# Optimization experiments

Hardware: AMD Instinct MI355X
Metric: run time of the kernel (lower is better)

The kernel has to match this reference:

```python
import jax, jax.numpy as jnp
import numpy as np

B, S, D, H = 2, 2048, 1024, 16
HD = D // H
NEG = -10000000000.0

def setup_inputs() -> dict:
    key = jax.random.key(0)
    ks = jax.random.split(key, 9)
    s = 1.0 / np.sqrt(D)
    return {
        "x": jax.random.normal(ks[0], (B, S, D), dtype=jnp.float32),
        "Wq": jax.random.uniform(ks[1], (D, D), jnp.float32, -s, s),
        "bq": jax.random.uniform(ks[2], (D,), jnp.float32, -s, s),
        "Wk": jax.random.uniform(ks[3], (D, D), jnp.float32, -s, s),
        "bk": jax.random.uniform(ks[4], (D,), jnp.float32, -s, s),
        "Wv": jax.random.uniform(ks[5], (D, D), jnp.float32, -s, s),
        "bv": jax.random.uniform(ks[6], (D,), jnp.float32, -s, s),
        "Wo": jax.random.uniform(ks[7], (D, D), jnp.float32, -s, s),
        "bo": jax.random.uniform(ks[8], (D,), jnp.float32, -s, s),
    }

def reference(x, Wq, bq, Wk, bk, Wv, bv, Wo, bo):
    b, s, _ = x.shape
    def split_heads(t):
        return t.reshape(b, s, H, HD).transpose(0, 2, 1, 3)  # [b,h,s,hd]
    Q = split_heads(x @ Wq + bq)
    K = split_heads(x @ Wk + bk)
    V = split_heads(x @ Wv + bv)
    scores = jnp.einsum('bhqd,bhkd->bhqk', Q, K) / jnp.sqrt(jnp.float32(HD))
    causal = jnp.tril(jnp.ones((s, s), dtype=bool))
    scores = jnp.where(causal[None, None], scores, NEG)
    attn = jax.nn.softmax(scores, axis=-1)
    ctx = jnp.einsum('bhqk,bhkd->bhqd', attn, V)
    ctx = ctx.transpose(0, 2, 1, 3).reshape(b, s, D)
    return ctx @ Wo + bo
```

## Files before the change

### kernel.cpp

```cpp
#include <hip/hip_runtime.h>
#include <hip/hip_bf16.h>

#define BB 2
#define SS 2048
#define DD 1024
#define HH 16
#define HD 64
#define MM (BB*SS)

typedef __attribute__((ext_vector_type(8))) short bf16x8;
typedef __attribute__((ext_vector_type(4))) float f32x4;
typedef __attribute__((ext_vector_type(16))) float f32x16;

#define QSCALE 0.18033688f

static __device__ __forceinline__ unsigned short f2bf(float f) {
    unsigned int u = __builtin_bit_cast(unsigned int, f);
    u += 0x7fffu + ((u >> 16) & 1u);
    return (unsigned short)(u >> 16);
}

static __device__ __forceinline__ void gload16(const unsigned short* g, unsigned short* l) {
    __builtin_amdgcn_global_load_lds(
        (const __attribute__((address_space(1))) unsigned int*)g,
        (__attribute__((address_space(3))) unsigned int*)l, 16, 0, 0);
}

__global__ __launch_bounds__(256) void prep_kernel(const float* __restrict__ x,
                                                   const float* __restrict__ W0,
                                                   const float* __restrict__ W1,
                                                   const float* __restrict__ W2,
                                                   const float* __restrict__ W3,
                                                   unsigned short* __restrict__ xb,
                                                   unsigned short* __restrict__ Wt)
{
    const int t = threadIdx.x;
    const int bid = blockIdx.x;
    if (bid < 2048) {
        const size_t i = ((size_t)bid * 256 + t) * 8;
        float4 a = *(const float4*)(x + i);
        float4 b = *(const float4*)(x + i + 4);
        union { unsigned short u[8]; bf16x8 v; } pk;
        pk.u[0] = f2bf(a.x); pk.u[1] = f2bf(a.y); pk.u[2] = f2bf(a.z); pk.u[3] = f2bf(a.w);
        pk.u[4] = f2bf(b.x); pk.u[5] = f2bf(b.y); pk.u[6] = f2bf(b.z); pk.u[7] = f2bf(b.w);
        *(bf16x8*)(xb + i) = pk.v;
        return;
    }
    __shared__ unsigned short Ts[64][72];
    const int wsel = (bid - 2048) >> 8;
    const int rem  = (bid - 2048) & 255;
    const float* W = wsel == 0 ? W0 : wsel == 1 ? W1 : wsel == 2 ? W2 : W3;
    unsigned short* out = Wt + (size_t)wsel * DD * DD;
    const int n0 = (rem & 15) * 64, k0 = (rem >> 4) * 64;
#pragma unroll
    for (int i = 0; i < 4; ++i) {
        const int r = (t >> 4) + i * 16;
        const int c = (t & 15) * 4;
        float4 v = *(const float4*)(W + (size_t)(k0 + r) * DD + n0 + c);
        Ts[c + 0][r] = f2bf(v.x); Ts[c + 1][r] = f2bf(v.y);
        Ts[c + 2][r] = f2bf(v.z); Ts[c + 3][r] = f2bf(v.w);
    }
    __syncthreads();
#pragma unroll
    for (int j = 0; j < 2; ++j) {
        const int ch = j * 256 + t;
        const int rn = ch >> 3, ck = (ch & 7) * 8;
        bf16x8 v = *(const bf16x8*)&Ts[rn][ck];
        *(bf16x8*)(out + (size_t)(n0 + rn) * DD + k0 + ck) = v;
    }
}

__global__ __launch_bounds__(256) void gemm_mfma(const unsigned short* __restrict__ A,
                                                 const unsigned short* __restrict__ Bt,
                                                 const float* __restrict__ bias0,
                                                 const float* __restrict__ bias1,
                                                 const float* __restrict__ bias2,
                                                 unsigned short* __restrict__ Qb,
                                                 unsigned short* __restrict__ Kb,
                                                 unsigned short* __restrict__ Vb,
                                                 float* __restrict__ outf,
                                                 int mode)
{
    __shared__ unsigned short As[2][128 * 64];
    __shared__ unsigned short Bs[2][128 * 64];

    const int t = threadIdx.x;
    const int w = t >> 6, l = t & 63;
    const int lane16 = l & 15, quad = l >> 4;
    const int m0 = blockIdx.x * 128, n0 = blockIdx.y * 128;
    const int wm = (w & 1) * 64, wn = (w >> 1) * 64;

    f32x4 acc[4][4] = {};

    int srow[4], skcg[4];
#pragma unroll
    for (int j = 0; j < 4; ++j) {
        const int c = t + j * 256;
        srow[j] = c >> 3;
        skcg[j] = (c & 7) ^ (srow[j] & 7);
    }

#pragma unroll
    for (int j = 0; j < 4; ++j) {
        const int c = t + j * 256;
        gload16(A  + (size_t)(m0 + srow[j]) * DD + skcg[j] * 8, &As[0][c * 8]);
        gload16(Bt + (size_t)(n0 + srow[j]) * DD + skcg[j] * 8, &Bs[0][c * 8]);
    }
    __syncthreads();

#pragma unroll 2
    for (int kt = 0; kt < 16; ++kt) {
        const int cur = kt & 1;
        if (kt + 1 < 16) {
            const int k1 = (kt + 1) * 64;
#pragma unroll
            for (int j = 0; j < 4; ++j) {
                const int c = t + j * 256;
                gload16(A  + (size_t)(m0 + srow[j]) * DD + k1 + skcg[j] * 8, &As[cur ^ 1][c * 8]);
                gload16(Bt + (size_t)(n0 + srow[j]) * DD + k1 + skcg[j] * 8, &Bs[cur ^ 1][c * 8]);
            }
        }
#pragma unroll
        for (int h = 0; h < 2; ++h) {
            bf16x8 af[4], bfr[4];
#pragma unroll
            for (int mt = 0; mt < 4; ++mt) {
                const int row = wm + mt * 16 + lane16;
                af[mt] = *(const bf16x8*)&As[cur][(row * 8 + ((h * 4 + quad) ^ (row & 7))) * 8];
            }
#pragma unroll
            for (int nt = 0; nt < 4; ++nt) {
                const int row = wn + nt * 16 + lane16;
                bfr[nt] = *(const bf16x8*)&Bs[cur][(row * 8 + ((h * 4 + quad) ^ (row & 7))) * 8];
            }
#pragma unroll
            for (int mt = 0; mt < 4; ++mt)
#pragma unroll
                for (int nt = 0; nt < 4; ++nt)
                    acc[mt][nt] = __builtin_amdgcn_mfma_f32_16x16x32_bf16(af[mt], bfr[nt], acc[mt][nt], 0, 0, 0);
        }
        __syncthreads();
    }

    if (mode == 0) {
        const int which = n0 >> 10;
        const float* bias = which == 0 ? bias0 : which == 1 ? bias1 : bias2;
#pragma unroll
        for (int nt = 0; nt < 4; ++nt) {
            const int gcol = n0 + wn + nt * 16 + lane16;
            const int cd = gcol & 1023;
            const float bv = bias[cd];
            const int h_ = cd >> 6, d = cd & 63;
            if (which == 2) {
#pragma unroll
                for (int mt = 0; mt < 4; ++mt) {
                    const int row0 = m0 + wm + mt * 16 + quad * 4;
                    const int b_ = row0 >> 11, s0 = row0 & 2047;
                    union { unsigned short u[4]; uint2 v; } pk;
#pragma unroll
                    for (int r = 0; r < 4; ++r) pk.u[r] = f2bf(acc[mt][nt][r] + bv);
                    *(uint2*)(Vb + ((size_t)(b_ * HH + h_) * HD + d) * SS + s0) = pk.v;
                }
            } else {
                unsigned short* dst3 = which == 0 ? Qb : Kb;
                const float sc_ = which == 0 ? QSCALE : 1.0f;
#pragma unroll
                for (int mt = 0; mt < 4; ++mt)
#pragma unroll
                    for (int r = 0; r < 4; ++r) {
                        const int row = m0 + wm + mt * 16 + quad * 4 + r;
                        const int b_ = row >> 11, s_ = row & 2047;
                        dst3[(((size_t)(b_ * HH + h_) * SS + s_) * HD) + d] =
                            f2bf((acc[mt][nt][r] + bv) * sc_);
                    }
            }
        }
    } else {
#pragma unroll
        for (int nt = 0; nt < 4; ++nt) {
            const int gcol = n0 + wn + nt * 16 + lane16;
            const float bv = bias0[gcol];
#pragma unroll
            for (int mt = 0; mt < 4; ++mt)
#pragma unroll
                for (int r = 0; r < 4; ++r) {
                    const int row = m0 + wm + mt * 16 + quad * 4 + r;
                    outf[(size_t)row * DD + gcol] = acc[mt][nt][r] + bv;
                }
        }
    }
}

__global__ __launch_bounds__(256) void attn_mfma(const unsigned short* __restrict__ Q,
                                                 const unsigned short* __restrict__ K,
                                                 const unsigned short* __restrict__ V,
                                                 unsigned short* __restrict__ ctx)
{
    __shared__ unsigned short Ks[2][4096];
    __shared__ unsigned short Vs[2][4096];

    const int t = threadIdx.x;
    const int w = t >> 6, l = t & 63;
    const int l31 = l & 31, hi = l >> 5;
    const int bid = blockIdx.x;
    const int halfg = bid >> 8, idx = bid & 255;
    const int qb_ = idx >> 5;
    const int qblk = halfg ? qb_ : 15 - qb_;
    const int hb = idx & 31;
    const int h = hb & 15, b = hb >> 4;
    const int q0 = qblk * 128;
    const size_t bh = (size_t)(b * HH + h) * SS;
    const unsigned short* Vg = V + (size_t)(b * HH + h) * HD * SS;

    const int wq0 = q0 + w * 32;
    bf16x8 qf[4];
#pragma unroll
    for (int dt = 0; dt < 4; ++dt)
        qf[dt] = *(const bf16x8*)(Q + (bh + wq0 + l31) * HD + dt * 16 + hi * 8);

    f32x16 ot[2] = {};
    float lp = 0.f;

    const int ntiles = 2 * qblk + 2;
    const int sr0 = t >> 3,          sg0 = (t & 7) ^ (sr0 & 7);
    const int sr1 = (t + 256) >> 3,  sg1 = ((t + 256) & 7) ^ (sr1 & 7);

    {
        gload16(K  + (bh + sr0) * HD + sg0 * 8,        &Ks[0][t * 8]);
        gload16(K  + (bh + sr1) * HD + sg1 * 8,        &Ks[0][(t + 256) * 8]);
        gload16(Vg + (size_t)sr0 * SS + sg0 * 8,       &Vs[0][t * 8]);
        gload16(Vg + (size_t)sr1 * SS + sg1 * 8,       &Vs[0][(t + 256) * 8]);
    }

    for (int kt = 0; kt < ntiles; ++kt) {
        __syncthreads();
        if (kt + 1 < ntiles) {
            const int k1 = (kt + 1) * 64;
            const int bi = (kt + 1) & 1;
            gload16(K  + (bh + k1 + sr0) * HD + sg0 * 8,   &Ks[bi][t * 8]);
            gload16(K  + (bh + k1 + sr1) * HD + sg1 * 8,   &Ks[bi][(t + 256) * 8]);
            gload16(Vg + (size_t)sr0 * SS + k1 + sg0 * 8,  &Vs[bi][t * 8]);
            gload16(Vg + (size_t)sr1 * SS + k1 + sg1 * 8,  &Vs[bi][(t + 256) * 8]);
        }
        const int k0 = kt * 64;
        if (k0 > wq0 + 31) continue;
        const unsigned short* Kt = Ks[kt & 1];
        const unsigned short* Vt = Vs[kt & 1];

        f32x16 s[2] = {};
#pragma unroll
        for (int dt = 0; dt < 4; ++dt) {
#pragma unroll
            for (int kh = 0; kh < 2; ++kh) {
                const int row = kh * 32 + l31;
                bf16x8 kf = *(const bf16x8*)&Kt[(row * 8 + ((dt * 2 + hi) ^ (row & 7))) * 8];
                s[kh] = __builtin_amdgcn_mfma_f32_32x32x16_bf16(kf, qf[dt], s[kh], 0, 0, 0);
            }
        }

        if (k0 + 63 > wq0) {
            const int q = wq0 + l31;
#pragma unroll
            for (int kh = 0; kh < 2; ++kh)
#pragma unroll
                for (int r = 0; r < 16; ++r) {
                    const int k = k0 + kh * 32 + (r & 3) + 8 * (r >> 2) + 4 * hi;
                    if (k > q) s[kh][r] = -1e30f;
                }
        }

#pragma unroll
        for (int kh = 0; kh < 2; ++kh) {
#pragma unroll
            for (int r = 0; r < 16; ++r) s[kh][r] = __builtin_amdgcn_exp2f(s[kh][r]);
            const float t0 = (s[kh][0] + s[kh][1]) + (s[kh][2] + s[kh][3]);
            const float t1 = (s[kh][4] + s[kh][5]) + (s[kh][6] + s[kh][7]);
            const float t2 = (s[kh][8] + s[kh][9]) + (s[kh][10] + s[kh][11]);
            const float t3 = (s[kh][12] + s[kh][13]) + (s[kh][14] + s[kh][15]);
            lp += (t0 + t1) + (t2 + t3);
        }

#pragma unroll
        for (int kh = 0; kh < 2; ++kh) {
#pragma unroll
            for (int c = 0; c < 2; ++c) {
                const int rb = c * 8;
                unsigned int w0, w1, w2, w3;
                asm("v_cvt_pk_bf16_f32 %0, %1, %2" : "=v"(w0) : "v"(s[kh][rb + 0]), "v"(s[kh][rb + 1]));
                asm("v_cvt_pk_bf16_f32 %0, %1, %2" : "=v"(w2) : "v"(s[kh][rb + 4]), "v"(s[kh][rb + 5]));
                asm("v_cvt_pk_bf16_f32 %0, %1, %2" : "=v"(w1) : "v"(s[kh][rb + 2]), "v"(s[kh][rb + 3]));
                asm("v_cvt_pk_bf16_f32 %0, %1, %2" : "=v"(w3) : "v"(s[kh][rb + 6]), "v"(s[kh][rb + 7]));
                asm("v_permlane32_swap_b32 %0, %1" : "+v"(w0), "+v"(w2));
                asm("v_permlane32_swap_b32 %0, %1" : "+v"(w1), "+v"(w3));
                union { unsigned int u[4]; bf16x8 v; } pa;
                pa.u[0] = w0; pa.u[1] = w1; pa.u[2] = w2; pa.u[3] = w3;
                const int chunk = kh * 4 + c * 2 + hi;
                const int rlo = l31, rhi2 = 32 + l31;
                bf16x8 v0 = *(const bf16x8*)&Vt[(rlo * 8 + (chunk ^ (rlo & 7))) * 8];
                bf16x8 v1 = *(const bf16x8*)&Vt[(rhi2 * 8 + (chunk ^ (rhi2 & 7))) * 8];
                ot[0] = __builtin_amdgcn_mfma_f32_32x32x16_bf16(v0, pa.v, ot[0], 0, 0, 0);
                ot[1] = __builtin_amdgcn_mfma_f32_32x32x16_bf16(v1, pa.v, ot[1], 0, 0, 0);
            }
        }
    }

    lp += __shfl_xor(lp, 32);
    const float inv = 1.f / lp;

    const int qrow = wq0 + l31;
    unsigned short* dst = ctx + ((size_t)(b * SS) + qrow) * DD + h * HD;
#pragma unroll
    for (int a2 = 0; a2 < 2; ++a2)
#pragma unroll
        for (int u = 0; u < 4; ++u) {
            const int d0 = a2 * 32 + 8 * u + 4 * hi;
            union { unsigned short u4[4]; uint2 v; } pk;
#pragma unroll
            for (int r = 0; r < 4; ++r) pk.u4[r] = f2bf(ot[a2][4 * u + r] * inv);
            *(uint2*)(dst + d0) = pk.v;
        }
}

extern "C" void kernel_launch(void* const* d_in, const int* in_sizes, int n_in,
                              void* d_out, int out_size, void* d_ws, size_t ws_size,
                              hipStream_t stream) {
    const float* x  = (const float*)d_in[0];
    const float* Wq = (const float*)d_in[1];
    const float* bq = (const float*)d_in[2];
    const float* Wk = (const float*)d_in[3];
    const float* bk = (const float*)d_in[4];
    const float* Wv = (const float*)d_in[5];
    const float* bv = (const float*)d_in[6];
    const float* Wo = (const float*)d_in[7];
    const float* bo = (const float*)d_in[8];
    float* out = (float*)d_out;

    unsigned short* xb  = (unsigned short*)d_ws;
    unsigned short* Wt  = xb  + (size_t)MM * DD;
    unsigned short* Qb  = Wt  + (size_t)4 * DD * DD;
    unsigned short* Kb  = Qb  + (size_t)MM * DD;
    unsigned short* Vb  = Kb  + (size_t)MM * DD;
    unsigned short* ctxb = Vb + (size_t)MM * DD;

    prep_kernel<<<2048 + 1024, 256, 0, stream>>>(x, Wq, Wk, Wv, Wo, xb, Wt);

    gemm_mfma<<<dim3(MM / 128, 3072 / 128), 256, 0, stream>>>(
        xb, Wt, bq, bk, bv, Qb, Kb, Vb, nullptr, 0);

    attn_mfma<<<(SS / 128) * HH * BB, 256, 0, stream>>>(Qb, Kb, Vb, ctxb);

    gemm_mfma<<<dim3(MM / 128, DD / 128), 256, 0, stream>>>(
        ctxb, Wt + (size_t)3 * DD * DD, bo, nullptr, nullptr,
        nullptr, nullptr, nullptr, out, 1);
}
```

Before: 190.2 us.

## Split attention KV tiles across two wave groups with 512-thread blocks

The attention kernel now launches 512 threads per block. Two groups of four waves process alternating 64-key tiles for the same 32-row query slices, using a 4-stage shared-memory ring that loads two tiles per superstep. At the end, partial outputs and row sums from the odd group are reduced through shared memory before normalization and store. This doubles the waves working on each query block to improve latency hiding and MFMA utilization. The cost is an extra reduction pass, double the LDS footprint, and load imbalance on the causal diagonal.

Result: faster. 183.3 us (-3.7%).

```diff
diff --git a/kernel.cpp b/kernel.cpp
--- a/kernel.cpp
+++ b/kernel.cpp
@@ -191,17 +191,18 @@
     }
 }
 
-__global__ __launch_bounds__(256) void attn_mfma(const unsigned short* __restrict__ Q,
+__global__ __launch_bounds__(512) void attn_mfma(const unsigned short* __restrict__ Q,
                                                  const unsigned short* __restrict__ K,
                                                  const unsigned short* __restrict__ V,
                                                  unsigned short* __restrict__ ctx)
 {
-    __shared__ unsigned short Ks[2][4096];
-    __shared__ unsigned short Vs[2][4096];
+    __shared__ unsigned short Ks[4][4096];
+    __shared__ unsigned short Vs[4][4096];
 
     const int t = threadIdx.x;
     const int w = t >> 6, l = t & 63;
     const int l31 = l & 31, hi = l >> 5;
+    const int qg = w & 3, par = w >> 2;
     const int bid = blockIdx.x;
     const int halfg = bid >> 8, idx = bid & 255;
     const int qb_ = idx >> 5;
@@ -212,7 +213,7 @@
     const size_t bh = (size_t)(b * HH + h) * SS;
     const unsigned short* Vg = V + (size_t)(b * HH + h) * HD * SS;
 
-    const int wq0 = q0 + w * 32;
+    const int wq0 = q0 + qg * 32;
     bf16x8 qf[4];
 #pragma unroll
     for (int dt = 0; dt < 4; ++dt)
@@ -222,103 +223,128 @@
     float lp = 0.f;
 
     const int ntiles = 2 * qblk + 2;
-    const int sr0 = t >> 3,          sg0 = (t & 7) ^ (sr0 & 7);
-    const int sr1 = (t + 256) >> 3,  sg1 = ((t + 256) & 7) ^ (sr1 & 7);
+    const int sr = t >> 3;
+    const int sg = (t & 7) ^ (sr & 7);
 
     {
-        gload16(K  + (bh + sr0) * HD + sg0 * 8,        &Ks[0][t * 8]);
-        gload16(K  + (bh + sr1) * HD + sg1 * 8,        &Ks[0][(t + 256) * 8]);
-        gload16(Vg + (size_t)sr0 * SS + sg0 * 8,       &Vs[0][t * 8]);
-        gload16(Vg + (size_t)sr1 * SS + sg1 * 8,       &Vs[0][(t + 256) * 8]);
-    }
-
-    for (int kt = 0; kt < ntiles; ++kt) {
+        gload16(K  + (bh + sr) * HD + sg * 8,            &Ks[0][t * 8]);
+        gload16(K  + (bh + 64 + sr) * HD + sg * 8,       &Ks[1][t * 8]);
+        gload16(Vg + (size_t)sr * SS + sg * 8,           &Vs[0][t * 8]);
+        gload16(Vg + (size_t)sr * SS + 64 + sg * 8,      &Vs[1][t * 8]);
+    }
+    __syncthreads();
+
+    const int nsup = ntiles >> 1;
+    for (int st = 0; st < nsup; ++st) {
+        if (2 * st + 2 < ntiles) {
+            const int ka = (2 * st + 2) * 64, kb = ka + 64;
+            const int ba = (2 * st + 2) & 3, bb2 = (2 * st + 3) & 3;
+            gload16(K  + (bh + ka + sr) * HD + sg * 8,       &Ks[ba][t * 8]);
+            gload16(K  + (bh + kb + sr) * HD + sg * 8,       &Ks[bb2][t * 8]);
+            gload16(Vg + (size_t)sr * SS + ka + sg * 8,      &Vs[ba][t * 8]);
+            gload16(Vg + (size_t)sr * SS + kb + sg * 8,      &Vs[bb2][t * 8]);
+        }
+
+        const int mt = 2 * st + par;
+        const int k0 = mt * 64;
+        if (k0 <= wq0 + 31) {
+            const unsigned short* Kt = Ks[mt & 3];
+            const unsigned short* Vt = Vs[mt & 3];
+
+            f32x16 s[2] = {};
+#pragma unroll
+            for (int dt = 0; dt < 4; ++dt) {
+#pragma unroll
+                for (int kh = 0; kh < 2; ++kh) {
+                    const int row = kh * 32 + l31;
+                    bf16x8 kf = *(const bf16x8*)&Kt[(row * 8 + ((dt * 2 + hi) ^ (row & 7))) * 8];
+                    s[kh] = __builtin_amdgcn_mfma_f32_32x32x16_bf16(kf, qf[dt], s[kh], 0, 0, 0);
+                }
+            }
+
+            if (k0 + 63 > wq0) {
+                const int q = wq0 + l31;
+#pragma unroll
+                for (int kh = 0; kh < 2; ++kh)
+#pragma unroll
+                    for (int r = 0; r < 16; ++r) {
+                        const int k = k0 + kh * 32 + (r & 3) + 8 * (r >> 2) + 4 * hi;
+                        if (k > q) s[kh][r] = -1e30f;
+                    }
+            }
+
+#pragma unroll
+            for (int kh = 0; kh < 2; ++kh) {
+#pragma unroll
+                for (int r = 0; r < 16; ++r) s[kh][r] = __builtin_amdgcn_exp2f(s[kh][r]);
+                const float t0 = (s[kh][0] + s[kh][1]) + (s[kh][2] + s[kh][3]);
+                const float t1 = (s[kh][4] + s[kh][5]) + (s[kh][6] + s[kh][7]);
+                const float t2 = (s[kh][8] + s[kh][9]) + (s[kh][10] + s[kh][11]);
+                const float t3 = (s[kh][12] + s[kh][13]) + (s[kh][14] + s[kh][15]);
+                lp += (t0 + t1) + (t2 + t3);
+            }
+
+#pragma unroll
+            for (int kh = 0; kh < 2; ++kh) {
+#pragma unroll
+                for (int c = 0; c < 2; ++c) {
+                    const int rb = c * 8;
+                    unsigned int w0, w1, w2, w3;
+                    asm("v_cvt_pk_bf16_f32 %0, %1, %2" : "=v"(w0) : "v"(s[kh][rb + 0]), "v"(s[kh][rb + 1]));
+                    asm("v_cvt_pk_bf16_f32 %0, %1, %2" : "=v"(w2) : "v"(s[kh][rb + 4]), "v"(s[kh][rb + 5]));
+                    asm("v_cvt_pk_bf16_f32 %0, %1, %2" : "=v"(w1) : "v"(s[kh][rb + 2]), "v"(s[kh][rb + 3]));
+                    asm("v_cvt_pk_bf16_f32 %0, %1, %2" : "=v"(w3) : "v"(s[kh][rb + 6]), "v"(s[kh][rb + 7]));
+                    asm("v_permlane32_swap_b32 %0, %1" : "+v"(w0), "+v"(w2));
+                    asm("v_permlane32_swap_b32 %0, %1" : "+v"(w1), "+v"(w3));
+                    union { unsigned int u[4]; bf16x8 v; } pa;
+                    pa.u[0] = w0; pa.u[1] = w1; pa.u[2] = w2; pa.u[3] = w3;
+                    const int chunk = kh * 4 + c * 2 + hi;
+                    const int rlo = l31, rhi2 = 32 + l31;
+                    bf16x8 v0 = *(const bf16x8*)&Vt[(rlo * 8 + (chunk ^ (rlo & 7))) * 8];
+                    bf16x8 v1 = *(const bf16x8*)&Vt[(rhi2 * 8 + (chunk ^ (rhi2 & 7))) * 8];
+                    ot[0] = __builtin_amdgcn_mfma_f32_32x32x16_bf16(v0, pa.v, ot[0], 0, 0, 0);
+                    ot[1] = __builtin_amdgcn_mfma_f32_32x32x16_bf16(v1, pa.v, ot[1], 0, 0, 0);
+                }
+            }
+        }
         __syncthreads();
-        if (kt + 1 < ntiles) {
-            const int k1 = (kt + 1) * 64;
-            const int bi = (kt + 1) & 1;
-            gload16(K  + (bh + k1 + sr0) * HD + sg0 * 8,   &Ks[bi][t * 8]);
-            gload16(K  + (bh + k1 + sr1) * HD + sg1 * 8,   &Ks[bi][(t + 256) * 8]);
-            gload16(Vg + (size_t)sr0 * SS + k1 + sg0 * 8,  &Vs[bi][t * 8]);
-            gload16(Vg + (size_t)sr1 * SS + k1 + sg1 * 8,  &Vs[bi][(t + 256) * 8]);
-        }
-        const int k0 = kt * 64;
-        if (k0 > wq0 + 31) continue;
-        const unsigned short* Kt = Ks[kt & 1];
-        const unsigned short* Vt = Vs[kt & 1];
-
-        f32x16 s[2] = {};
-#pragma unroll
-        for (int dt = 0; dt < 4; ++dt) {
-#pragma unroll
-            for (int kh = 0; kh < 2; ++kh) {
-                const int row = kh * 32 + l31;
-                bf16x8 kf = *(const bf16x8*)&Kt[(row * 8 + ((dt * 2 + hi) ^ (row & 7))) * 8];
-                s[kh] = __builtin_amdgcn_mfma_f32_32x32x16_bf16(kf, qf[dt], s[kh], 0, 0, 0);
-            }
-        }
-
-        if (k0 + 63 > wq0) {
-            const int q = wq0 + l31;
-#pragma unroll
-            for (int kh = 0; kh < 2; ++kh)
-#pragma unroll
-                for (int r = 0; r < 16; ++r) {
-                    const int k = k0 + kh * 32 + (r & 3) + 8 * (r >> 2) + 4 * hi;
-                    if (k > q) s[kh][r] = -1e30f;
-                }
-        }
-
-#pragma unroll
-        for (int kh = 0; kh < 2; ++kh) {
-#pragma unroll
-            for (int r = 0; r < 16; ++r) s[kh][r] = __builtin_amdgcn_exp2f(s[kh][r]);
-            const float t0 = (s[kh][0] + s[kh][1]) + (s[kh][2] + s[kh][3]);
-            const float t1 = (s[kh][4] + s[kh][5]) + (s[kh][6] + s[kh][7]);
-            const float t2 = (s[kh][8] + s[kh][9]) + (s[kh][10] + s[kh][11]);
-            const float t3 = (s[kh][12] + s[kh][13]) + (s[kh][14] + s[kh][15]);
-            lp += (t0 + t1) + (t2 + t3);
-        }
-
-#pragma unroll
-        for (int kh = 0; kh < 2; ++kh) {
-#pragma unroll
-            for (int c = 0; c < 2; ++c) {
-                const int rb = c * 8;
-                unsigned int w0, w1, w2, w3;
-                asm("v_cvt_pk_bf16_f32 %0, %1, %2" : "=v"(w0) : "v"(s[kh][rb + 0]), "v"(s[kh][rb + 1]));
-                asm("v_cvt_pk_bf16_f32 %0, %1, %2" : "=v"(w2) : "v"(s[kh][rb + 4]), "v"(s[kh][rb + 5]));
-                asm("v_cvt_pk_bf16_f32 %0, %1, %2" : "=v"(w1) : "v"(s[kh][rb + 2]), "v"(s[kh][rb + 3]));
-                asm("v_cvt_pk_bf16_f32 %0, %1, %2" : "=v"(w3) : "v"(s[kh][rb + 6]), "v"(s[kh][rb + 7]));
-                asm("v_permlane32_swap_b32 %0, %1" : "+v"(w0), "+v"(w2));
-                asm("v_permlane32_swap_b32 %0, %1" : "+v"(w1), "+v"(w3));
-                union { unsigned int u[4]; bf16x8 v; } pa;
-                pa.u[0] = w0; pa.u[1] = w1; pa.u[2] = w2; pa.u[3] = w3;
-                const int chunk = kh * 4 + c * 2 + hi;
-                const int rlo = l31, rhi2 = 32 + l31;
-                bf16x8 v0 = *(const bf16x8*)&Vt[(rlo * 8 + (chunk ^ (rlo & 7))) * 8];
-                bf16x8 v1 = *(const bf16x8*)&Vt[(rhi2 * 8 + (chunk ^ (rhi2 & 7))) * 8];
-                ot[0] = __builtin_amdgcn_mfma_f32_32x32x16_bf16(v0, pa.v, ot[0], 0, 0, 0);
-                ot[1] = __builtin_amdgcn_mfma_f32_32x32x16_bf16(v1, pa.v, ot[1], 0, 0, 0);
-            }
-        }
-    }
-
-    lp += __shfl_xor(lp, 32);
-    const float inv = 1.f / lp;
-
-    const int qrow = wq0 + l31;
-    unsigned short* dst = ctx + ((size_t)(b * SS) + qrow) * DD + h * HD;
-#pragma unroll
-    for (int a2 = 0; a2 < 2; ++a2)
-#pragma unroll
-        for (int u = 0; u < 4; ++u) {
-            const int d0 = a2 * 32 + 8 * u + 4 * hi;
-            union { unsigned short u4[4]; uint2 v; } pk;
-#pragma unroll
-            for (int r = 0; r < 4; ++r) pk.u4[r] = f2bf(ot[a2][4 * u + r] * inv);
-            *(uint2*)(dst + d0) = pk.v;
-        }
+    }
+
+    float* Osh = (float*)&Ks[0][0];
+    float* Lsh = (float*)&Vs[0][0];
+    if (par == 1) {
+        float* o = Osh + qg * 2048;
+#pragma unroll
+        for (int a2 = 0; a2 < 2; ++a2)
+#pragma unroll
+            for (int r = 0; r < 16; ++r) o[(a2 * 16 + r) * 64 + l] = ot[a2][r];
+        Lsh[qg * 64 + l] = lp;
+    }
+    __syncthreads();
+    if (par == 0) {
+        float* o = Osh + qg * 2048;
+#pragma unroll
+        for (int a2 = 0; a2 < 2; ++a2)
+#pragma unroll
+            for (int r = 0; r < 16; ++r) ot[a2][r] += o[(a2 * 16 + r) * 64 + l];
+        lp += Lsh[qg * 64 + l];
+
+        lp += __shfl_xor(lp, 32);
+        const float inv = 1.f / lp;
+
+        const int qrow = wq0 + l31;
+        unsigned short* dst = ctx + ((size_t)(b * SS) + qrow) * DD + h * HD;
+#pragma unroll
+        for (int a2 = 0; a2 < 2; ++a2)
+#pragma unroll
+            for (int u = 0; u < 4; ++u) {
+                const int d0 = a2 * 32 + 8 * u + 4 * hi;
+                union { unsigned short u4[4]; uint2 v; } pk;
+#pragma unroll
+                for (int r = 0; r < 4; ++r) pk.u4[r] = f2bf(ot[a2][4 * u + r] * inv);
+                *(uint2*)(dst + d0) = pk.v;
+            }
+    }
 }
 
 extern "C" void kernel_launch(void* const* d_in, const int* in_sizes, int n_in,
@@ -347,7 +373,7 @@
     gemm_mfma<<<dim3(MM / 128, 3072 / 128), 256, 0, stream>>>(
         xb, Wt, bq, bk, bv, Qb, Kb, Vb, nullptr, 0);
 
-    attn_mfma<<<(SS / 128) * HH * BB, 256, 0, stream>>>(Qb, Kb, Vb, ctxb);
+    attn_mfma<<<(SS / 128) * HH * BB, 512, 0, stream>>>(Qb, Kb, Vb, ctxb);
 
     gemm_mfma<<<dim3(MM / 128, DD / 128), 256, 0, stream>>>(
         ctxb, Wt + (size_t)3 * DD * DD, bo, nullptr, nullptr,
```
